# Optimization experiments

Measured on AMD Instinct MI355X. Metric: run time of the kernel, lower is better.

The kernel has to match this reference:

```python
import jax, jax.numpy as jnp
import numpy as np

MAXV = 8  # convex quad clipped by 4 half-planes has <= 8 vertices


def decode(enc, anchors):
    """ResidualCoder.decode_torch for 7-dof lidar boxes (x,y,z,dx,dy,dz,r)."""
    xa, ya, za, dxa, dya, dza, ra = [anchors[..., i] for i in range(7)]
    xt, yt, zt, dxt, dyt, dzt, rt = [enc[..., i] for i in range(7)]
    diag = jnp.sqrt(dxa * dxa + dya * dya)
    xg = xt * diag + xa
    yg = yt * diag + ya
    zg = zt * dza + za
    dxg = jnp.exp(dxt) * dxa
    dyg = jnp.exp(dyt) * dya
    dzg = jnp.exp(dzt) * dza
    rg = rt + ra
    return jnp.stack([xg, yg, zg, dxg, dyg, dzg, rg], axis=-1)


def bev_corners(boxes):
    # boxes (...,7) -> CCW BEV corners (...,4,2) using x,y,dx,dy,heading
    x, y, dx, dy, r = boxes[..., 0], boxes[..., 1], boxes[..., 3], boxes[..., 4], boxes[..., 6]
    cx = jnp.stack([dx, -dx, -dx, dx], -1) * 0.5
    cy = jnp.stack([dy, dy, -dy, -dy], -1) * 0.5
    c, s = jnp.cos(r)[..., None], jnp.sin(r)[..., None]
    px = cx * c - cy * s + x[..., None]
    py = cx * s + cy * c + y[..., None]
    return jnp.stack([px, py], -1)


def _clip(poly, n, A, B):
    """Sutherland-Hodgman clip of polygon (poly[:n]) by half-plane left of A->B."""
    idx = jnp.arange(MAXV)
    e = B - A
    s = e[0] * (poly[:, 1] - A[1]) - e[1] * (poly[:, 0] - A[0])  # signed side
    prev = (idx - 1) % jnp.maximum(n, 1)
    s_prev = s[prev]
    p_prev = poly[prev]
    active = idx < n
    cin = s >= 0
    pin = s_prev >= 0
    den = s_prev - s
    t = s_prev / jnp.where(den == 0, 1.0, den)
    inter = p_prev + t[:, None] * (poly - p_prev)
    f_int = active & (cin != pin)   # edge crosses boundary -> emit intersection
    f_cur = active & cin            # current vertex inside -> emit it
    cand = jnp.stack([inter, poly], 1).reshape(2 * MAXV, 2)
    flags = jnp.stack([f_int, f_cur], 1).reshape(2 * MAXV)
    pos = jnp.cumsum(flags) - 1
    new_n = pos[-1] + 1
    pos = jnp.where(flags, pos, MAXV)  # invalid -> dump slot
    out = jnp.zeros((MAXV + 1, 2), poly.dtype).at[pos].set(cand)[:MAXV]
    return out, new_n.astype(jnp.int32)


def _pair_iou_bev(c1, c2, a1, a2):
    # c1,c2: (4,2) CCW corners of the two rotated BEV boxes; a1,a2: scalar areas
    poly = jnp.zeros((MAXV, 2), c1.dtype).at[:4].set(c1)
    n = jnp.asarray(4, jnp.int32)
    for e in range(4):
        poly, n = _clip(poly, n, c2[e], c2[(e + 1) % 4])
    idx = jnp.arange(MAXV)
    nxt = (idx + 1) % jnp.maximum(n, 1)
    x, y = poly[:, 0], poly[:, 1]
    contrib = jnp.where(idx < n, x * y[nxt] - x[nxt] * y, 0.0)
    inter = 0.5 * jnp.abs(contrib.sum())
    return inter / jnp.clip(a1 + a2 - inter, 1e-6, None)


def rotated_iou_bev_diag(boxes1, boxes2):
    """Diagonal (elementwise) rotated BEV IoU for flattened (M,7) lidar boxes."""
    c1 = bev_corners(boxes1)
    c2 = bev_corners(boxes2)
    a1 = boxes1[..., 3] * boxes1[..., 4]
    a2 = boxes2[..., 3] * boxes2[..., 4]
    return jax.vmap(_pair_iou_bev)(c1, c2, a1, a2)


def setup_inputs() -> dict:
    key = jax.random.key(0)
    ks = jax.random.split(key, 8)
    B, N = 4, 262144
    iou_preds = jax.random.normal(ks[0], (B, N), jnp.float32)
    one_hot_targets = jax.random.randint(ks[1], (B, N), 0, 2, jnp.int32)
    weights = jax.random.uniform(ks[2], (B, N), jnp.float32)
    # realistic anchors: xy in [-50,50], z ~ -1, dims in [1.5,4.5], heading in [0,pi)
    xy = jax.random.uniform(ks[3], (N, 2), jnp.float32, -50.0, 50.0)
    z = jnp.full((N, 1), -1.0, jnp.float32)
    dims = jax.random.uniform(ks[4], (N, 3), jnp.float32, 1.5, 4.5)
    ang = jax.random.uniform(ks[5], (N, 1), jnp.float32, 0.0, np.pi)
    anchors = jnp.concatenate([xy, z, dims, ang], axis=-1)
    box_preds = 0.1 * jax.random.normal(ks[6], (B, N, 7), jnp.float32)
    reg_targets = 0.1 * jax.random.normal(ks[7], (B, N, 7), jnp.float32)
    return {"iou_preds": iou_preds, "one_hot_targets": one_hot_targets,
            "weights": weights, "anchors": anchors,
            "box_preds": box_preds, "reg_targets": reg_targets}


def reference(iou_preds, one_hot_targets, weights, anchors, box_preds, reg_targets):
    B, N = iou_preds.shape
    dec_pred = decode(box_preds, anchors[None, :, :])   # (B,N,7)
    dec_tgt = decode(reg_targets, anchors[None, :, :])  # (B,N,7)
    iou = rotated_iou_bev_diag(dec_pred.reshape(B * N, 7),
                               dec_tgt.reshape(B * N, 7)).reshape(B, N)
    # label is computed with no grad, only at positive anchors; zero elsewhere
    target = jax.lax.stop_gradient(jnp.where(one_hot_targets > 0, iou, 0.0))
    # faithful to the original quirk: BCE-with-logits applied to sigmoid(iou_preds)
    z = jax.nn.sigmoid(iou_preds)
    p_t = jnp.logaddexp(0.0, z) - z * target  # log(1+e^z) - t*z
    return p_t * weights
```

## Files before the change

### kernel.cpp

```cpp
#include <hip/hip_runtime.h>
#include <math.h>

#define BLK 256


__device__ __forceinline__ float clamp_mag(float x) {
    return copysignf(fmaxf(fabsf(x), 1e-30f), x);
}

__device__ __forceinline__ void edge_piece(float px, float py, float ex, float ey,
                                           float rx, float ry, float hx, float hy,
                                           float& area2, float& Dx, float& Dy)
{
    float sx0 = (-hx - px) * rx, sx1 = (hx - px) * rx;
    float sy0 = (-hy - py) * ry, sy1 = (hy - py) * ry;
    float smin = fmaxf(fmaxf(fminf(sx0, sx1), fminf(sy0, sy1)), 0.0f);
    float smax = fminf(fminf(fmaxf(sx0, sx1), fmaxf(sy0, sy1)), 1.0f);
    smax = fmaxf(smax, smin);
    float ax = fmaf(smin, ex, px), ay = fmaf(smin, ey, py);
    float bx = fmaf(smax, ex, px), by = fmaf(smax, ey, py);
    float ux = bx - ax, uy = by - ay;
    area2 += fmaf(ax, uy, -(ay * ux));
    Dx += ux; Dy += uy;
}

__device__ __forceinline__ float pair_loss(const float bp[5], const float rt[5],
                                           float xa, float ya, float dxa, float dya,
                                           float ra, float diag,
                                           float ip, int oh, float w)
{
    float x1  = fmaf(bp[0], diag, xa);
    float y1  = fmaf(bp[1], diag, ya);
    float dx1 = __expf(bp[2]) * dxa;
    float dy1 = __expf(bp[3]) * dya;
    float r1  = bp[4] + ra;

    float x2  = fmaf(rt[0], diag, xa);
    float y2  = fmaf(rt[1], diag, ya);
    float dx2 = __expf(rt[2]) * dxa;
    float dy2 = __expf(rt[3]) * dya;
    float r2  = rt[4] + ra;

    float a1 = dx1 * dy1, a2 = dx2 * dy2;
    float h1x = 0.5f * dx1, h1y = 0.5f * dy1;
    float h2x = 0.5f * dx2, h2y = 0.5f * dy2;

    float c2v = __cosf(r2), s2v = __sinf(r2);
    float dr  = r1 - r2;
    float cd  = __cosf(dr), sd = __sinf(dr);
    float ddx = x1 - x2, ddy = y1 - y2;
    float tx  = fmaf(c2v, ddx,  s2v * ddy);
    float ty  = fmaf(-s2v, ddx, c2v * ddy);

    float ux_ = h1x * cd,  uy_ = h1x * sd;
    float vx_ = -h1y * sd, vy_ = h1y * cd;
    float eux = 2.0f * ux_, euy = 2.0f * uy_;
    float evx = 2.0f * vx_, evy = 2.0f * vy_;
    float ruxP = __fdividef(1.0f, clamp_mag(eux));
    float ruyP = __fdividef(1.0f, clamp_mag(euy));
    float rvxP = __fdividef(1.0f, clamp_mag(evx));
    float rvyP = __fdividef(1.0f, clamp_mag(evy));
    float p0x = tx + ux_ + vx_, p0y = ty + uy_ + vy_;
    float p1x = tx - ux_ + vx_, p1y = ty - uy_ + vy_;
    float p2x = tx - ux_ - vx_, p2y = ty - uy_ - vy_;
    float p3x = tx + ux_ - vx_, p3y = ty + uy_ - vy_;

    float area2 = 0.0f, dDx = 0.0f, dDy = 0.0f;
    edge_piece(p0x, p0y, -eux, -euy, -ruxP, -ruyP, h2x, h2y, area2, dDx, dDy);
    edge_piece(p1x, p1y, -evx, -evy, -rvxP, -rvyP, h2x, h2y, area2, dDx, dDy);
    edge_piece(p2x, p2y,  eux,  euy,  ruxP,  ruyP, h2x, h2y, area2, dDx, dDy);
    edge_piece(p3x, p3y,  evx,  evy,  rvxP,  rvyP, h2x, h2y, area2, dDx, dDy);

    float upx = h2x * cd,  upy = -h2x * sd;
    float vpx = h2y * sd,  vpy = h2y * cd;
    float ox  = -(fmaf(cd, tx,  sd * ty));
    float oy  = -(fmaf(-sd, tx, cd * ty));
    float equx = 2.0f * upx, equy = 2.0f * upy;
    float eqvx = 2.0f * vpx, eqvy = 2.0f * vpy;
    float ruxQ = __fdividef(1.0f, clamp_mag(equx));
    float ruyQ = __fdividef(1.0f, clamp_mag(equy));
    float rvxQ = __fdividef(1.0f, clamp_mag(eqvx));
    float rvyQ = __fdividef(1.0f, clamp_mag(eqvy));
    float q0x = ox + upx + vpx, q0y = oy + upy + vpy;
    float q1x = ox - upx + vpx, q1y = oy - upy + vpy;
    float q2x = ox - upx - vpx, q2y = oy - upy - vpy;
    float q3x = ox + upx - vpx, q3y = oy + upy - vpy;

    float Dx = 0.0f, Dy = 0.0f;
    edge_piece(q0x, q0y, -equx, -equy, -ruxQ, -ruyQ, h1x, h1y, area2, Dx, Dy);
    edge_piece(q1x, q1y, -eqvx, -eqvy, -rvxQ, -rvyQ, h1x, h1y, area2, Dx, Dy);
    edge_piece(q2x, q2y,  equx,  equy,  ruxQ,  ruyQ, h1x, h1y, area2, Dx, Dy);
    edge_piece(q3x, q3y,  eqvx,  eqvy,  rvxQ,  rvyQ, h1x, h1y, area2, Dx, Dy);

    float RDx = fmaf(cd, Dx, -(sd * Dy));
    float RDy = fmaf(sd, Dx,   cd * Dy);
    area2 += fmaf(tx, RDy, -(ty * RDx));

    float inter = 0.5f * fabsf(area2);
    float uni = fmaxf(a1 + a2 - inter, 1e-6f);
    float iou = __fdividef(inter, uni);

    float target = (oh > 0) ? iou : 0.0f;
    float z  = __fdividef(1.0f, 1.0f + __expf(-ip));
    float pt = __logf(1.0f + __expf(z)) - z * target;
    return pt * w;
}

__global__ __launch_bounds__(BLK)
void iou_pred_loss_kernel(const float* __restrict__ iou_preds,
                          const int*   __restrict__ one_hot,
                          const float* __restrict__ weights,
                          const float* __restrict__ anchors,
                          const float* __restrict__ box_preds,
                          const float* __restrict__ reg_targets,
                          float* __restrict__ out,
                          int N, int B)
{
    int tid   = threadIdx.x;
    int n_idx = blockIdx.x * BLK + tid;
    if (n_idx >= N) return;

    int yspan = gridDim.y;
    int b0 = blockIdx.y;
    int b1 = blockIdx.y + yspan;
    bool has2 = (b1 < B);
    size_t g0 = (size_t)b0 * N + n_idx;
    size_t g1 = (size_t)(has2 ? b1 : b0) * N + n_idx;

    const float* an = anchors + (size_t)n_idx * 7;
    float xa = an[0], ya = an[1], dxa = an[3], dya = an[4], ra = an[6];

    const float* bpp0 = box_preds   + g0 * 7;
    const float* rtp0 = reg_targets + g0 * 7;
    const float* bpp1 = box_preds   + g1 * 7;
    const float* rtp1 = reg_targets + g1 * 7;
    float bp0[5] = {bpp0[0], bpp0[1], bpp0[3], bpp0[4], bpp0[6]};
    float rt0[5] = {rtp0[0], rtp0[1], rtp0[3], rtp0[4], rtp0[6]};
    float bp1[5] = {bpp1[0], bpp1[1], bpp1[3], bpp1[4], bpp1[6]};
    float rt1[5] = {rtp1[0], rtp1[1], rtp1[3], rtp1[4], rtp1[6]};
    float ip0 = iou_preds[g0], ip1 = iou_preds[g1];
    int   oh0 = one_hot[g0],   oh1 = one_hot[g1];
    float w0  = weights[g0],   w1  = weights[g1];

    float diag = sqrtf(fmaf(dxa, dxa, dya * dya));

    out[g0] = pair_loss(bp0, rt0, xa, ya, dxa, dya, ra, diag, ip0, oh0, w0);
    if (has2)
        out[g1] = pair_loss(bp1, rt1, xa, ya, dxa, dya, ra, diag, ip1, oh1, w1);
}

extern "C" void kernel_launch(void* const* d_in, const int* in_sizes, int n_in,
                              void* d_out, int out_size, void* d_ws, size_t ws_size,
                              hipStream_t stream) {
    const float* iou_preds   = (const float*)d_in[0];
    const int*   one_hot     = (const int*)  d_in[1];
    const float* weights     = (const float*)d_in[2];
    const float* anchors     = (const float*)d_in[3];
    const float* box_preds   = (const float*)d_in[4];
    const float* reg_targets = (const float*)d_in[5];
    float* out = (float*)d_out;

    int total = in_sizes[0];
    int N     = in_sizes[3] / 7;
    int B     = total / N;

    dim3 grid((N + BLK - 1) / BLK, (B + 1) / 2);
    iou_pred_loss_kernel<<<grid, dim3(BLK), 0, stream>>>(
        iou_preds, one_hot, weights, anchors, box_preds, reg_targets,
        out, N, B);
}
```

Measured before the change: 111.4 us.

## Process four consecutive anchors per thread with float4 vectorized loads

```diff
diff --git a/kernel.cpp b/kernel.cpp
--- a/kernel.cpp
+++ b/kernel.cpp
@@ -2,6 +2,7 @@
 #include <math.h>
 
 #define BLK 256
+#define RPT 4
 
 
 __device__ __forceinline__ float clamp_mag(float x) {
@@ -116,37 +117,67 @@
                           float* __restrict__ out,
                           int N, int B)
 {
-    int tid   = threadIdx.x;
-    int n_idx = blockIdx.x * BLK + tid;
-    if (n_idx >= N) return;
-
-    int yspan = gridDim.y;
-    int b0 = blockIdx.y;
-    int b1 = blockIdx.y + yspan;
-    bool has2 = (b1 < B);
-    size_t g0 = (size_t)b0 * N + n_idx;
-    size_t g1 = (size_t)(has2 ? b1 : b0) * N + n_idx;
-
-    const float* an = anchors + (size_t)n_idx * 7;
-    float xa = an[0], ya = an[1], dxa = an[3], dya = an[4], ra = an[6];
-
-    const float* bpp0 = box_preds   + g0 * 7;
-    const float* rtp0 = reg_targets + g0 * 7;
-    const float* bpp1 = box_preds   + g1 * 7;
-    const float* rtp1 = reg_targets + g1 * 7;
-    float bp0[5] = {bpp0[0], bpp0[1], bpp0[3], bpp0[4], bpp0[6]};
-    float rt0[5] = {rtp0[0], rtp0[1], rtp0[3], rtp0[4], rtp0[6]};
-    float bp1[5] = {bpp1[0], bpp1[1], bpp1[3], bpp1[4], bpp1[6]};
-    float rt1[5] = {rtp1[0], rtp1[1], rtp1[3], rtp1[4], rtp1[6]};
-    float ip0 = iou_preds[g0], ip1 = iou_preds[g1];
-    int   oh0 = one_hot[g0],   oh1 = one_hot[g1];
-    float w0  = weights[g0],   w1  = weights[g1];
-
-    float diag = sqrtf(fmaf(dxa, dxa, dya * dya));
-
-    out[g0] = pair_loss(bp0, rt0, xa, ya, dxa, dya, ra, diag, ip0, oh0, w0);
-    if (has2)
-        out[g1] = pair_loss(bp1, rt1, xa, ya, dxa, dya, ra, diag, ip1, oh1, w1);
+    int tid  = threadIdx.x;
+    int row0 = (blockIdx.x * BLK + tid) * RPT;
+    if (row0 >= N) return;
+    int b = blockIdx.y;
+    size_t g0 = (size_t)b * N + row0;
+
+    if (row0 + RPT <= N) {
+        const float4* bp4 = (const float4*)(box_preds   + g0 * 7);
+        const float4* rt4 = (const float4*)(reg_targets + g0 * 7);
+        const float4* an4 = (const float4*)(anchors + (size_t)row0 * 7);
+
+        float fb[28], fr[28], fa[28];
+        #pragma unroll
+        for (int k = 0; k < 7; ++k) {
+            float4 t = bp4[k];
+            fb[4*k+0] = t.x; fb[4*k+1] = t.y; fb[4*k+2] = t.z; fb[4*k+3] = t.w;
+        }
+        #pragma unroll
+        for (int k = 0; k < 7; ++k) {
+            float4 t = rt4[k];
+            fr[4*k+0] = t.x; fr[4*k+1] = t.y; fr[4*k+2] = t.z; fr[4*k+3] = t.w;
+        }
+        #pragma unroll
+        for (int k = 0; k < 7; ++k) {
+            float4 t = an4[k];
+            fa[4*k+0] = t.x; fa[4*k+1] = t.y; fa[4*k+2] = t.z; fa[4*k+3] = t.w;
+        }
+        float4 ip4 = *(const float4*)(iou_preds + g0);
+        int4   oh4 = *(const int4*)  (one_hot   + g0);
+        float4 w4  = *(const float4*)(weights   + g0);
+        float ipv[RPT] = {ip4.x, ip4.y, ip4.z, ip4.w};
+        int   ohv[RPT] = {oh4.x, oh4.y, oh4.z, oh4.w};
+        float wv[RPT]  = {w4.x,  w4.y,  w4.z,  w4.w};
+
+        float res[RPT];
+        #pragma unroll
+        for (int r = 0; r < RPT; ++r) {
+            float xa  = fa[7*r+0], ya  = fa[7*r+1];
+            float dxa = fa[7*r+3], dya = fa[7*r+4], ra = fa[7*r+6];
+            float diag = sqrtf(fmaf(dxa, dxa, dya * dya));
+            float bp[5] = {fb[7*r+0], fb[7*r+1], fb[7*r+3], fb[7*r+4], fb[7*r+6]};
+            float rt[5] = {fr[7*r+0], fr[7*r+1], fr[7*r+3], fr[7*r+4], fr[7*r+6]};
+            res[r] = pair_loss(bp, rt, xa, ya, dxa, dya, ra, diag,
+                               ipv[r], ohv[r], wv[r]);
+        }
+        float4 o = {res[0], res[1], res[2], res[3]};
+        *(float4*)(out + g0) = o;
+    } else {
+        for (int r = 0; r < RPT && row0 + r < N; ++r) {
+            size_t g = g0 + r;
+            const float* bpp = box_preds   + g * 7;
+            const float* rtp = reg_targets + g * 7;
+            const float* an  = anchors + (size_t)(row0 + r) * 7;
+            float bp[5] = {bpp[0], bpp[1], bpp[3], bpp[4], bpp[6]};
+            float rt[5] = {rtp[0], rtp[1], rtp[3], rtp[4], rtp[6]};
+            float xa = an[0], ya = an[1], dxa = an[3], dya = an[4], ra = an[6];
+            float diag = sqrtf(fmaf(dxa, dxa, dya * dya));
+            out[g] = pair_loss(bp, rt, xa, ya, dxa, dya, ra, diag,
+                               iou_preds[g], one_hot[g], weights[g]);
+        }
+    }
 }
 
 extern "C" void kernel_launch(void* const* d_in, const int* in_sizes, int n_in,
@@ -164,7 +195,8 @@
     int N     = in_sizes[3] / 7;
     int B     = total / N;
 
-    dim3 grid((N + BLK - 1) / BLK, (B + 1) / 2);
+    int rows_per_block = BLK * RPT;
+    dim3 grid((N + rows_per_block - 1) / rows_per_block, B);
     iou_pred_loss_kernel<<<grid, dim3(BLK), 0, stream>>>(
         iou_preds, one_hot, weights, anchors, box_preds, reg_targets,
         out, N, B);
```

Measured after the change: 127.2 us. +14.2%, slower.

## Stage AoS box rows through LDS with coalesced float4 loads per wave

Applied to the files above, without the earlier changes.

```diff
diff --git a/kernel.cpp b/kernel.cpp
--- a/kernel.cpp
+++ b/kernel.cpp
@@ -2,6 +2,9 @@
 #include <math.h>
 
 #define BLK 256
+#define WVS (BLK / 64)
+#define TW  448
+#define NARR 5
 
 
 __device__ __forceinline__ float clamp_mag(float x) {
@@ -116,37 +119,94 @@
                           float* __restrict__ out,
                           int N, int B)
 {
-    int tid   = threadIdx.x;
-    int n_idx = blockIdx.x * BLK + tid;
-    if (n_idx >= N) return;
+    __shared__ float s_lds[WVS * NARR * TW];
+
+    int tid  = threadIdx.x;
+    int lane = tid & 63;
+    int wid  = tid >> 6;
 
     int yspan = gridDim.y;
     int b0 = blockIdx.y;
     int b1 = blockIdx.y + yspan;
     bool has2 = (b1 < B);
-    size_t g0 = (size_t)b0 * N + n_idx;
-    size_t g1 = (size_t)(has2 ? b1 : b0) * N + n_idx;
-
-    const float* an = anchors + (size_t)n_idx * 7;
-    float xa = an[0], ya = an[1], dxa = an[3], dya = an[4], ra = an[6];
-
-    const float* bpp0 = box_preds   + g0 * 7;
-    const float* rtp0 = reg_targets + g0 * 7;
-    const float* bpp1 = box_preds   + g1 * 7;
-    const float* rtp1 = reg_targets + g1 * 7;
-    float bp0[5] = {bpp0[0], bpp0[1], bpp0[3], bpp0[4], bpp0[6]};
-    float rt0[5] = {rtp0[0], rtp0[1], rtp0[3], rtp0[4], rtp0[6]};
-    float bp1[5] = {bpp1[0], bpp1[1], bpp1[3], bpp1[4], bpp1[6]};
-    float rt1[5] = {rtp1[0], rtp1[1], rtp1[3], rtp1[4], rtp1[6]};
-    float ip0 = iou_preds[g0], ip1 = iou_preds[g1];
-    int   oh0 = one_hot[g0],   oh1 = one_hot[g1];
-    float w0  = weights[g0],   w1  = weights[g1];
-
-    float diag = sqrtf(fmaf(dxa, dxa, dya * dya));
-
-    out[g0] = pair_loss(bp0, rt0, xa, ya, dxa, dya, ra, diag, ip0, oh0, w0);
-    if (has2)
-        out[g1] = pair_loss(bp1, rt1, xa, ya, dxa, dya, ra, diag, ip1, oh1, w1);
+    int b1c = has2 ? b1 : b0;
+
+    int n_idx = blockIdx.x * BLK + tid;
+    bool full_block = (blockIdx.x * BLK + BLK) <= N;
+
+    if (full_block) {
+        int wrow0 = blockIdx.x * BLK + wid * 64;
+
+        const float4* pb0 = (const float4*)(box_preds   + ((size_t)b0  * N + wrow0) * 7);
+        const float4* pr0 = (const float4*)(reg_targets + ((size_t)b0  * N + wrow0) * 7);
+        const float4* pb1 = (const float4*)(box_preds   + ((size_t)b1c * N + wrow0) * 7);
+        const float4* pr1 = (const float4*)(reg_targets + ((size_t)b1c * N + wrow0) * 7);
+        const float4* pan = (const float4*)(anchors     + ((size_t)wrow0) * 7);
+
+        bool second = lane < (TW / 4 - 64);
+        int  l2 = 64 + lane;
+
+        float4 a0 = pb0[lane], a1 = pr0[lane], a2 = pb1[lane], a3 = pr1[lane], a4 = pan[lane];
+        float4 c0, c1, c2, c3, c4;
+        if (second) { c0 = pb0[l2]; c1 = pr0[l2]; c2 = pb1[l2]; c3 = pr1[l2]; c4 = pan[l2]; }
+
+        size_t g0 = (size_t)b0  * N + n_idx;
+        size_t g1 = (size_t)b1c * N + n_idx;
+        float ip0 = iou_preds[g0], ip1 = iou_preds[g1];
+        int   oh0 = one_hot[g0],   oh1 = one_hot[g1];
+        float w0  = weights[g0],   w1  = weights[g1];
+
+        float4* t0 = (float4*)&s_lds[(wid * NARR + 0) * TW];
+        float4* t1 = (float4*)&s_lds[(wid * NARR + 1) * TW];
+        float4* t2 = (float4*)&s_lds[(wid * NARR + 2) * TW];
+        float4* t3 = (float4*)&s_lds[(wid * NARR + 3) * TW];
+        float4* t4 = (float4*)&s_lds[(wid * NARR + 4) * TW];
+        t0[lane] = a0; t1[lane] = a1; t2[lane] = a2; t3[lane] = a3; t4[lane] = a4;
+        if (second) { t0[l2] = c0; t1[l2] = c1; t2[l2] = c2; t3[l2] = c3; t4[l2] = c4; }
+
+        int lw = lane * 7;
+        const float* f0 = &s_lds[(wid * NARR + 0) * TW];
+        const float* f1 = &s_lds[(wid * NARR + 1) * TW];
+        const float* f2 = &s_lds[(wid * NARR + 2) * TW];
+        const float* f3 = &s_lds[(wid * NARR + 3) * TW];
+        const float* f4 = &s_lds[(wid * NARR + 4) * TW];
+
+        float xa = f4[lw + 0], ya = f4[lw + 1];
+        float dxa = f4[lw + 3], dya = f4[lw + 4], ra = f4[lw + 6];
+        float diag = sqrtf(fmaf(dxa, dxa, dya * dya));
+
+        {
+            float bp[5] = { f0[lw+0], f0[lw+1], f0[lw+3], f0[lw+4], f0[lw+6] };
+            float rt[5] = { f1[lw+0], f1[lw+1], f1[lw+3], f1[lw+4], f1[lw+6] };
+            out[g0] = pair_loss(bp, rt, xa, ya, dxa, dya, ra, diag, ip0, oh0, w0);
+        }
+        if (has2) {
+            float bp[5] = { f2[lw+0], f2[lw+1], f2[lw+3], f2[lw+4], f2[lw+6] };
+            float rt[5] = { f3[lw+0], f3[lw+1], f3[lw+3], f3[lw+4], f3[lw+6] };
+            out[g1] = pair_loss(bp, rt, xa, ya, dxa, dya, ra, diag, ip1, oh1, w1);
+        }
+    } else if (n_idx < N) {
+        size_t g0 = (size_t)b0  * N + n_idx;
+        size_t g1 = (size_t)b1c * N + n_idx;
+        const float* an = anchors + (size_t)n_idx * 7;
+        float xa = an[0], ya = an[1], dxa = an[3], dya = an[4], ra = an[6];
+        float diag = sqrtf(fmaf(dxa, dxa, dya * dya));
+
+        const float* bpp0 = box_preds   + g0 * 7;
+        const float* rtp0 = reg_targets + g0 * 7;
+        float bp0[5] = {bpp0[0], bpp0[1], bpp0[3], bpp0[4], bpp0[6]};
+        float rt0[5] = {rtp0[0], rtp0[1], rtp0[3], rtp0[4], rtp0[6]};
+        out[g0] = pair_loss(bp0, rt0, xa, ya, dxa, dya, ra, diag,
+                            iou_preds[g0], one_hot[g0], weights[g0]);
+        if (has2) {
+            const float* bpp1 = box_preds   + g1 * 7;
+            const float* rtp1 = reg_targets + g1 * 7;
+            float bp1[5] = {bpp1[0], bpp1[1], bpp1[3], bpp1[4], bpp1[6]};
+            float rt1[5] = {rtp1[0], rtp1[1], rtp1[3], rtp1[4], rtp1[6]};
+            out[g1] = pair_loss(bp1, rt1, xa, ya, dxa, dya, ra, diag,
+                                iou_preds[g1], one_hot[g1], weights[g1]);
+        }
+    }
 }
 
 extern "C" void kernel_launch(void* const* d_in, const int* in_sizes, int n_in,
```

Result: no change. 113.1 us (+1.5%).
